# Optimization experiments

Hardware: AMD Instinct MI355X
Metric: run time of the kernel (lower is better)

Reference implementation:

```python
import jax, jax.numpy as jnp
import numpy as np

B, N, D = 4, 1024, 1024
H = 16
DH = D // H  # 64
DROPOUT_P = 0.5


def setup_inputs() -> dict:
    key = jax.random.key(0)
    ks = jax.random.split(key, 6)
    query = jax.random.normal(ks[0], (B, N, D), dtype=jnp.float32)
    key_t = jax.random.normal(ks[1], (B, N, D), dtype=jnp.float32)
    value = jax.random.normal(ks[2], (B, N, D), dtype=jnp.float32)
    # torch Linear(D, 3D): weight [3D, D], bias [3D]
    W_qkv = jax.random.normal(ks[3], (3 * D, D), dtype=jnp.float32) * (1.0 / np.sqrt(D))
    b_qkv = jax.random.normal(ks[4], (3 * D,), dtype=jnp.float32) * 0.01
    # inverted dropout mask: keep_prob = 1 - p, kept entries scaled by 1/keep
    keep = 1.0 - DROPOUT_P
    drop_mask = (jax.random.uniform(ks[5], (B * H, N, N)) < keep).astype(jnp.float32) / keep
    return {"query": query, "key": key_t, "value": value,
            "W_qkv": W_qkv, "b_qkv": b_qkv, "drop_mask": drop_mask}


def _split_heads(t):
    # 'b n (h d) -> (b h) n d'
    b, n, _ = t.shape
    return t.reshape(b, n, H, DH).transpose(0, 2, 1, 3).reshape(b * H, n, DH)


def reference(query, key, value, W_qkv, b_qkv, drop_mask):
    # key/value args are unused by the original module (it derives q,k,v from query)
    qkv = query @ W_qkv.T + b_qkv                      # [b, n, 3d]
    q, k, v = jnp.split(qkv, 3, axis=-1)
    q, k, v = _split_heads(q), _split_heads(k), _split_heads(v)  # [(b h), n, dh]
    qk = jnp.einsum('znd,zmd->znm', q, k)              # [(b h), n, n]
    # faithful quirk: original does qk.div(1/sqrt(dh)) == qk * sqrt(dh)
    scaled_qk = qk * jnp.sqrt(jnp.float32(DH))
    attn = jax.nn.softmax(scaled_qk, axis=-1)
    attn = attn * drop_mask                            # deterministic inverted dropout
    out = jnp.einsum('znm,zmd->znd', attn, v)          # [(b h), n, dh]
    # '(b h) n d -> b n (h d)'
    out = out.reshape(B, H, N, DH).transpose(0, 2, 1, 3).reshape(B, N, D)
    return out
```

## Files before the change

kernel.cpp:

```cpp
#include <hip/hip_runtime.h>


typedef _Float16 f16;
typedef _Float16 f16x4 __attribute__((ext_vector_type(4)));
typedef _Float16 f16x8 __attribute__((ext_vector_type(8)));
typedef float    f32x4 __attribute__((ext_vector_type(4)));

#define MFMA16(a, b, c) __builtin_amdgcn_mfma_f32_16x16x32_f16((a), (b), (c), 0, 0, 0)

__device__ __forceinline__ void gll16(const f16* g, f16* l) {
  __builtin_amdgcn_global_load_lds(
      (const __attribute__((address_space(1))) unsigned int*)g,
      (__attribute__((address_space(3))) unsigned int*)l, 16, 0, 0);
}

__device__ __forceinline__ f16x8 ldsfrag(const f16* tile, int row, int chunk) {
  return *(const f16x8*)&tile[row * 64 + ((chunk ^ (row & 7)) << 3)];
}

__global__ __launch_bounds__(256) void cvt_split(const float4* __restrict__ s,
                                                 f16x4* __restrict__ hi,
                                                 f16x4* __restrict__ lo, int n4) {
  int i = blockIdx.x * 256 + threadIdx.x;
  if (i >= n4) return;
  float4 v = s[i];
  f16x4 h, l;
  h[0] = (f16)v.x; l[0] = (f16)(v.x - (float)h[0]);
  h[1] = (f16)v.y; l[1] = (f16)(v.y - (float)h[1]);
  h[2] = (f16)v.z; l[2] = (f16)(v.z - (float)h[2]);
  h[3] = (f16)v.w; l[3] = (f16)(v.w - (float)h[3]);
  hi[i] = h; lo[i] = l;
}

__global__ __launch_bounds__(256) void proj_gemm(
    const f16* __restrict__ qh, const f16* __restrict__ ql,
    const f16* __restrict__ wh, const f16* __restrict__ wl,
    const float* __restrict__ bias,
    f16* __restrict__ Qh, f16* __restrict__ Ql,
    f16* __restrict__ Kh, f16* __restrict__ Kl,
    f16* __restrict__ Vh) {
  __shared__ f16 Ah[128 * 32], Al[128 * 32], Bh[128 * 32], Bl[128 * 32];
  const int tid = threadIdx.x;
  const int bid = blockIdx.x;
  const int wg = (bid & 7) * 96 + (bid >> 3);
  const int m0 = (wg / 24) * 128, n0 = (wg % 24) * 128;
  const bool isv = (n0 >= 2048);
  const int wid = tid >> 6, lane = tid & 63;
  const int wm = (wid >> 1) * 64, wn = (wid & 1) * 64;
  const int r16 = lane & 15, g = lane >> 4;

  f32x4 zero4 = {0.f, 0.f, 0.f, 0.f};
  f32x4 acc[4][4];
#pragma unroll
  for (int i = 0; i < 4; ++i)
#pragma unroll
    for (int j = 0; j < 4; ++j) acc[i][j] = zero4;

  for (int s = 0; s < 32; ++s) {
    const int kk = s << 5;
    const f16* Abh = qh + (size_t)m0 * 1024 + kk;
    const f16* Abl = ql + (size_t)m0 * 1024 + kk;
    const f16* Bbh = wh + (size_t)n0 * 1024 + kk;
    const f16* Bbl = wl + (size_t)n0 * 1024 + kk;
#pragma unroll
    for (int it = 0; it < 2; ++it) {
      const int c = tid + it * 256;
      const int go = (c >> 2) * 1024 + (c & 3) * 8;
      gll16(Abh + go, &Ah[c * 8]);
      gll16(Bbh + go, &Bh[c * 8]);
      if (!isv) {
        gll16(Abl + go, &Al[c * 8]);
        gll16(Bbl + go, &Bl[c * 8]);
      }
    }
    __syncthreads();
    f16x8 a[4], al_[4];
#pragma unroll
    for (int i = 0; i < 4; ++i) {
      a[i] = *(const f16x8*)&Ah[(wm + i * 16 + r16) * 32 + g * 8];
      if (!isv) al_[i] = *(const f16x8*)&Al[(wm + i * 16 + r16) * 32 + g * 8];
    }
#pragma unroll
    for (int j = 0; j < 4; ++j) {
      const f16x8 b = *(const f16x8*)&Bh[(wn + j * 16 + r16) * 32 + g * 8];
      if (!isv) {
        const f16x8 bl = *(const f16x8*)&Bl[(wn + j * 16 + r16) * 32 + g * 8];
#pragma unroll
        for (int i = 0; i < 4; ++i) {
          acc[i][j] = MFMA16(a[i], b, acc[i][j]);
          acc[i][j] = MFMA16(al_[i], b, acc[i][j]);
          acc[i][j] = MFMA16(a[i], bl, acc[i][j]);
        }
      } else {
#pragma unroll
        for (int i = 0; i < 4; ++i) acc[i][j] = MFMA16(a[i], b, acc[i][j]);
      }
    }
    __syncthreads();
  }

#pragma unroll
  for (int j = 0; j < 4; ++j) {
    const int col = n0 + wn + j * 16 + r16;
    const float bv = bias[col];
#pragma unroll
    for (int i = 0; i < 4; ++i) {
#pragma unroll
      for (int rr = 0; rr < 4; ++rr) {
        const int m = m0 + wm + i * 16 + g * 4 + rr;
        const float c = acc[i][j][rr] + bv;
        const int bi = m >> 10, n = m & 1023;
        if (col < 1024) {
          const int z = bi * 16 + (col >> 6), dh = col & 63;
          const size_t idx = ((size_t)z * 1024 + n) * 64 + dh;
          f16 h = (f16)c;
          Qh[idx] = h; Ql[idx] = (f16)(c - (float)h);
        } else if (col < 2048) {
          const int c2 = col - 1024;
          const int z = bi * 16 + (c2 >> 6), dh = c2 & 63;
          const size_t idx = ((size_t)z * 1024 + n) * 64 + dh;
          f16 h = (f16)c;
          Kh[idx] = h; Kl[idx] = (f16)(c - (float)h);
        } else {
          const int c2 = col - 2048;
          const int z = bi * 16 + (c2 >> 6), dh = c2 & 63;
          Vh[((size_t)z * 1024 + n) * 64 + dh] = (f16)c;
        }
      }
    }
  }
}

__global__ __launch_bounds__(256) void transp_v(const f16* __restrict__ Vh,
                                                f16* __restrict__ Vt) {
  __shared__ f16 t[64][80];
  const int z = blockIdx.y, nt = blockIdx.x;
  const int tid = threadIdx.x;
#pragma unroll
  for (int it = 0; it < 2; ++it) {
    int c = tid + it * 256;
    int row = c >> 3, cc = c & 7;
    *(f16x8*)&t[row][cc * 8] =
        *(const f16x8*)&Vh[(((size_t)z << 10) + nt * 64 + row) * 64 + cc * 8];
  }
  __syncthreads();
#pragma unroll
  for (int it = 0; it < 2; ++it) {
    int c = tid + it * 256;
    int dh = c >> 3, ncc = c & 7;
    f16x8 o;
#pragma unroll
    for (int j = 0; j < 8; ++j) o[j] = t[ncc * 8 + j][dh];
    *(f16x8*)&Vt[((size_t)z * 64 + dh) * 1024 + nt * 64 + ncc * 8] = o;
  }
}

__global__ __launch_bounds__(512) void attn(
    const f16* __restrict__ Qh_, const f16* __restrict__ Ql_,
    const f16* __restrict__ Kh_, const f16* __restrict__ Kl_,
    const f16* __restrict__ Vt_, const float* __restrict__ mask,
    float* __restrict__ out) {
  __shared__ f16 Khs[2][4096], Kls[2][4096], Vts[2][4096];
  __shared__ f16 Ps[8][1024];

  const int bid = blockIdx.x;
  const int wg = (bid & 7) * 64 + (bid >> 3);
  const int qt = wg & 7, z = wg >> 3;
  const int q0 = qt * 128;
  const int tid = threadIdx.x, w = tid >> 6, lane = tid & 63;
  const int r16 = lane & 15, g = lane >> 4;

  const size_t zrow = (size_t)z << 10;
  const f16* qrh = Qh_ + (zrow + q0 + w * 16 + r16) * 64;
  const f16* qrl = Ql_ + (zrow + q0 + w * 16 + r16) * 64;
  f16x8 qa[2], qla[2];
#pragma unroll
  for (int ks = 0; ks < 2; ++ks) {
    qa[ks] = *(const f16x8*)&qrh[ks * 32 + g * 8];
    qla[ks] = *(const f16x8*)&qrl[ks * 32 + g * 8];
  }

  const f16* KzhB = Kh_ + zrow * 64;
  const f16* KzlB = Kl_ + zrow * 64;
  const f16* VzB = Vt_ + (size_t)z * 64 * 1024;
  const int sc = tid, srow = sc >> 3, ssc = ((sc & 7) ^ (srow & 7)) << 3;

#define STAGE(buf, k0_)                                                   \
  do {                                                                    \
    gll16(KzhB + (size_t)((k0_) + srow) * 64 + ssc, &Khs[buf][sc * 8]);   \
    gll16(KzlB + (size_t)((k0_) + srow) * 64 + ssc, &Kls[buf][sc * 8]);   \
    gll16(VzB + (size_t)srow * 1024 + (k0_) + ssc, &Vts[buf][sc * 8]);    \
  } while (0)

  STAGE(0, 0);

  float mrow[4] = {-1e30f, -1e30f, -1e30f, -1e30f};
  float lrow[4] = {0.f, 0.f, 0.f, 0.f};
  f32x4 zero4 = {0.f, 0.f, 0.f, 0.f};
  f32x4 acc[4];
#pragma unroll
  for (int df = 0; df < 4; ++df) acc[df] = zero4;

  const float* mz = mask + ((size_t)z << 20);
  const int qrow_m = q0 + w * 16 + g * 4;
  f16* Pw = &Ps[w][0];
  __syncthreads();

  for (int kt = 0; kt < 16; ++kt) {
    const int cur = kt & 1;
    const int k0 = kt << 6;
    if (kt < 15) STAGE(cur ^ 1, k0 + 64);

    float mv[4][4];
#pragma unroll
    for (int cf = 0; cf < 4; ++cf)
#pragma unroll
      for (int rr = 0; rr < 4; ++rr)
        mv[cf][rr] = mz[(size_t)(qrow_m + rr) * 1024 + k0 + cf * 16 + r16];

    __builtin_amdgcn_s_setprio(1);
    f32x4 s[4];
#pragma unroll
    for (int cf = 0; cf < 4; ++cf) {
      const int krow = cf * 16 + r16;
      const f16x8 kh0 = ldsfrag(&Khs[cur][0], krow, g);
      const f16x8 kh1 = ldsfrag(&Khs[cur][0], krow, 4 + g);
      const f16x8 kl0 = ldsfrag(&Kls[cur][0], krow, g);
      const f16x8 kl1 = ldsfrag(&Kls[cur][0], krow, 4 + g);
      f32x4 t = zero4;
      t = MFMA16(qa[0], kh0, t);
      t = MFMA16(qla[0], kh0, t);
      t = MFMA16(qa[0], kl0, t);
      t = MFMA16(qa[1], kh1, t);
      t = MFMA16(qla[1], kh1, t);
      t = MFMA16(qa[1], kl1, t);
      s[cf] = t;
    }
    __builtin_amdgcn_s_setprio(0);

    float s8[4][4];
#pragma unroll
    for (int cf = 0; cf < 4; ++cf)
#pragma unroll
      for (int rr = 0; rr < 4; ++rr) s8[cf][rr] = s[cf][rr] * 8.0f;

    float rm[4];
#pragma unroll
    for (int rr = 0; rr < 4; ++rr)
      rm[rr] = fmaxf(fmaxf(s8[0][rr], s8[1][rr]), fmaxf(s8[2][rr], s8[3][rr]));
#pragma unroll
    for (int mk = 1; mk < 16; mk <<= 1)
#pragma unroll
      for (int rr = 0; rr < 4; ++rr)
        rm[rr] = fmaxf(rm[rr], __shfl_xor(rm[rr], mk, 64));

    float mnew[4], scal[4];
#pragma unroll
    for (int rr = 0; rr < 4; ++rr) {
      mnew[rr] = fmaxf(mrow[rr], rm[rr]);
      scal[rr] = __expf(mrow[rr] - mnew[rr]);
      mrow[rr] = mnew[rr];
    }

    float p_[4][4], rs[4] = {0.f, 0.f, 0.f, 0.f};
#pragma unroll
    for (int cf = 0; cf < 4; ++cf)
#pragma unroll
      for (int rr = 0; rr < 4; ++rr) {
        p_[cf][rr] = __expf(s8[cf][rr] - mnew[rr]);
        rs[rr] += p_[cf][rr];
      }
#pragma unroll
    for (int mk = 1; mk < 16; mk <<= 1)
#pragma unroll
      for (int rr = 0; rr < 4; ++rr) rs[rr] += __shfl_xor(rs[rr], mk, 64);
#pragma unroll
    for (int rr = 0; rr < 4; ++rr) lrow[rr] = lrow[rr] * scal[rr] + rs[rr];
#pragma unroll
    for (int df = 0; df < 4; ++df)
#pragma unroll
      for (int rr = 0; rr < 4; ++rr) acc[df][rr] *= scal[rr];

#pragma unroll
    for (int cf = 0; cf < 4; ++cf)
#pragma unroll
      for (int rr = 0; rr < 4; ++rr) {
        const int prow = g * 4 + rr, key = cf * 16 + r16;
        Pw[prow * 64 + (((key >> 3) ^ (prow & 7)) << 3) + (key & 7)] =
            (f16)(p_[cf][rr] * mv[cf][rr]);
      }
    f16x8 pf[2];
#pragma unroll
    for (int ks2 = 0; ks2 < 2; ++ks2)
      pf[ks2] = ldsfrag(Pw, r16, ks2 * 4 + g);

    __builtin_amdgcn_s_setprio(1);
#pragma unroll
    for (int df = 0; df < 4; ++df)
#pragma unroll
      for (int ks2 = 0; ks2 < 2; ++ks2)
        acc[df] = MFMA16(pf[ks2],
                         ldsfrag(&Vts[cur][0], df * 16 + r16, ks2 * 4 + g),
                         acc[df]);
    __builtin_amdgcn_s_setprio(0);
    __syncthreads();
  }

  const int bi = z >> 4, hh = z & 15;
#pragma unroll
  for (int df = 0; df < 4; ++df)
#pragma unroll
    for (int rr = 0; rr < 4; ++rr) {
      const int n = q0 + w * 16 + g * 4 + rr;
      out[((size_t)bi * 1024 + n) * 1024 + hh * 64 + df * 16 + r16] =
          acc[df][rr] / lrow[rr];
    }
#undef STAGE
}

extern "C" void kernel_launch(void* const* d_in, const int* in_sizes, int n_in,
                              void* d_out, int out_size, void* d_ws,
                              size_t ws_size, hipStream_t stream) {
  const float* query = (const float*)d_in[0];
  const float* W = (const float*)d_in[3];
  const float* bias = (const float*)d_in[4];
  const float* mask = (const float*)d_in[5];
  float* out = (float*)d_out;

  f16* p = (f16*)d_ws;
  f16* qh = p;              p += (size_t)4096 * 1024;
  f16* ql = p;              p += (size_t)4096 * 1024;
  f16* wh = p;              p += (size_t)3072 * 1024;
  f16* wl = p;              p += (size_t)3072 * 1024;
  f16* Qh = p;              p += (size_t)64 * 1024 * 64;
  f16* Ql = p;              p += (size_t)64 * 1024 * 64;
  f16* Kh = p;              p += (size_t)64 * 1024 * 64;
  f16* Kl = p;              p += (size_t)64 * 1024 * 64;
  f16* Vh = p;              p += (size_t)64 * 1024 * 64;
  f16* Vt = p;

  cvt_split<<<(1048576 + 255) / 256, 256, 0, stream>>>(
      (const float4*)query, (f16x4*)qh, (f16x4*)ql, 1048576);
  cvt_split<<<(786432 + 255) / 256, 256, 0, stream>>>(
      (const float4*)W, (f16x4*)wh, (f16x4*)wl, 786432);
  proj_gemm<<<768, 256, 0, stream>>>(qh, ql, wh, wl, bias, Qh, Ql, Kh, Kl, Vh);
  transp_v<<<dim3(16, 64), 256, 0, stream>>>(Vh, Vt);
  attn<<<512, 512, 0, stream>>>(Qh, Ql, Kh, Kl, Vt, mask, out);
}
```

Baseline: 561.8 us.

## Pack dropout mask to bits and streamline online softmax in attention

A new pre-pass packs the float dropout mask into one bit per element, so the attention kernel reads a single 64-bit word per row per key tile instead of sixteen scattered floats per lane. The QK MFMA operands are swapped so each lane owns a whole query row, which removes most cross-lane shuffles for the row max and row sum. Rescaling of the running max is skipped unless the max grows by more than a threshold, and P is written to LDS as packed 4-wide vectors. The kept value is hardcoded as 2·p, which assumes the mask only holds 0 or 1/keep with keep = 0.5. The full mask is still read once per call, now in a separate extra kernel launch.

```diff
diff --git a/kernel.cpp b/kernel.cpp
--- a/kernel.cpp
+++ b/kernel.cpp
@@ -5,6 +5,8 @@
 typedef _Float16 f16x4 __attribute__((ext_vector_type(4)));
 typedef _Float16 f16x8 __attribute__((ext_vector_type(8)));
 typedef float    f32x4 __attribute__((ext_vector_type(4)));
+typedef unsigned long long u64;
+typedef unsigned short u16;
 
 #define MFMA16(a, b, c) __builtin_amdgcn_mfma_f32_16x16x32_f16((a), (b), (c), 0, 0, 0)
 
@@ -30,6 +32,25 @@
   h[2] = (f16)v.z; l[2] = (f16)(v.z - (float)h[2]);
   h[3] = (f16)v.w; l[3] = (f16)(v.w - (float)h[3]);
   hi[i] = h; lo[i] = l;
+}
+
+__global__ __launch_bounds__(256) void mask_bits(const float4* __restrict__ mask,
+                                                 u16* __restrict__ bits16) {
+  const size_t t = (size_t)blockIdx.x * 256 + threadIdx.x;
+  const float4 v0 = mask[t * 4 + 0];
+  const float4 v1 = mask[t * 4 + 1];
+  const float4 v2 = mask[t * 4 + 2];
+  const float4 v3 = mask[t * 4 + 3];
+  unsigned m = 0;
+  m |= (v0.x > 1.f) ? 0x0001u : 0u;  m |= (v0.y > 1.f) ? 0x0002u : 0u;
+  m |= (v0.z > 1.f) ? 0x0004u : 0u;  m |= (v0.w > 1.f) ? 0x0008u : 0u;
+  m |= (v1.x > 1.f) ? 0x0010u : 0u;  m |= (v1.y > 1.f) ? 0x0020u : 0u;
+  m |= (v1.z > 1.f) ? 0x0040u : 0u;  m |= (v1.w > 1.f) ? 0x0080u : 0u;
+  m |= (v2.x > 1.f) ? 0x0100u : 0u;  m |= (v2.y > 1.f) ? 0x0200u : 0u;
+  m |= (v2.z > 1.f) ? 0x0400u : 0u;  m |= (v2.w > 1.f) ? 0x0800u : 0u;
+  m |= (v3.x > 1.f) ? 0x1000u : 0u;  m |= (v3.y > 1.f) ? 0x2000u : 0u;
+  m |= (v3.z > 1.f) ? 0x4000u : 0u;  m |= (v3.w > 1.f) ? 0x8000u : 0u;
+  bits16[t] = (u16)m;
 }
 
 __global__ __launch_bounds__(256) void proj_gemm(
@@ -158,7 +179,7 @@
 __global__ __launch_bounds__(512) void attn(
     const f16* __restrict__ Qh_, const f16* __restrict__ Ql_,
     const f16* __restrict__ Kh_, const f16* __restrict__ Kl_,
-    const f16* __restrict__ Vt_, const float* __restrict__ mask,
+    const f16* __restrict__ Vt_, const u64* __restrict__ bits,
     float* __restrict__ out) {
   __shared__ f16 Khs[2][4096], Kls[2][4096], Vts[2][4096];
   __shared__ f16 Ps[8][1024];
@@ -194,16 +215,16 @@
 
   STAGE(0, 0);
 
-  float mrow[4] = {-1e30f, -1e30f, -1e30f, -1e30f};
-  float lrow[4] = {0.f, 0.f, 0.f, 0.f};
+  float mrow = -1e30f, lrow = 0.f;
   f32x4 zero4 = {0.f, 0.f, 0.f, 0.f};
   f32x4 acc[4];
 #pragma unroll
   for (int df = 0; df < 4; ++df) acc[df] = zero4;
 
-  const float* mz = mask + ((size_t)z << 20);
-  const int qrow_m = q0 + w * 16 + g * 4;
+  const u64* browp = bits + (zrow + q0 + w * 16 + r16) * 16;
   f16* Pw = &Ps[w][0];
+  f16* pwbase = Pw + r16 * 64 + (g & 1) * 4;
+  const int pswz = r16 & 7, ghalf = g >> 1;
   __syncthreads();
 
   for (int kt = 0; kt < 16; ++kt) {
@@ -211,12 +232,7 @@
     const int k0 = kt << 6;
     if (kt < 15) STAGE(cur ^ 1, k0 + 64);
 
-    float mv[4][4];
-#pragma unroll
-    for (int cf = 0; cf < 4; ++cf)
-#pragma unroll
-      for (int rr = 0; rr < 4; ++rr)
-        mv[cf][rr] = mz[(size_t)(qrow_m + rr) * 1024 + k0 + cf * 16 + r16];
+    const u64 bm = browp[kt];
 
     __builtin_amdgcn_s_setprio(1);
     f32x4 s[4];
@@ -228,12 +244,12 @@
       const f16x8 kl0 = ldsfrag(&Kls[cur][0], krow, g);
       const f16x8 kl1 = ldsfrag(&Kls[cur][0], krow, 4 + g);
       f32x4 t = zero4;
-      t = MFMA16(qa[0], kh0, t);
-      t = MFMA16(qla[0], kh0, t);
-      t = MFMA16(qa[0], kl0, t);
-      t = MFMA16(qa[1], kh1, t);
-      t = MFMA16(qla[1], kh1, t);
-      t = MFMA16(qa[1], kl1, t);
+      t = MFMA16(kh0, qa[0], t);
+      t = MFMA16(kh0, qla[0], t);
+      t = MFMA16(kl0, qa[0], t);
+      t = MFMA16(kh1, qa[1], t);
+      t = MFMA16(kh1, qla[1], t);
+      t = MFMA16(kl1, qa[1], t);
       s[cf] = t;
     }
     __builtin_amdgcn_s_setprio(0);
@@ -244,51 +260,50 @@
 #pragma unroll
       for (int rr = 0; rr < 4; ++rr) s8[cf][rr] = s[cf][rr] * 8.0f;
 
-    float rm[4];
-#pragma unroll
-    for (int rr = 0; rr < 4; ++rr)
-      rm[rr] = fmaxf(fmaxf(s8[0][rr], s8[1][rr]), fmaxf(s8[2][rr], s8[3][rr]));
-#pragma unroll
-    for (int mk = 1; mk < 16; mk <<= 1)
-#pragma unroll
-      for (int rr = 0; rr < 4; ++rr)
-        rm[rr] = fmaxf(rm[rr], __shfl_xor(rm[rr], mk, 64));
-
-    float mnew[4], scal[4];
-#pragma unroll
-    for (int rr = 0; rr < 4; ++rr) {
-      mnew[rr] = fmaxf(mrow[rr], rm[rr]);
-      scal[rr] = __expf(mrow[rr] - mnew[rr]);
-      mrow[rr] = mnew[rr];
-    }
-
-    float p_[4][4], rs[4] = {0.f, 0.f, 0.f, 0.f};
+    float m16 = s8[0][0];
 #pragma unroll
     for (int cf = 0; cf < 4; ++cf)
 #pragma unroll
+      for (int rr = 0; rr < 4; ++rr) m16 = fmaxf(m16, s8[cf][rr]);
+    m16 = fmaxf(m16, __shfl_xor(m16, 16, 64));
+    m16 = fmaxf(m16, __shfl_xor(m16, 32, 64));
+
+    if (!__all(m16 <= mrow + 8.f)) {
+      const float mnew = fmaxf(mrow, m16);
+      const float scal = __expf(mrow - mnew);
+      mrow = mnew;
+      lrow *= scal;
+      float sq[4];
+#pragma unroll
+      for (int rr = 0; rr < 4; ++rr) sq[rr] = __shfl(scal, g * 4 + rr, 16);
+#pragma unroll
+      for (int df = 0; df < 4; ++df)
+#pragma unroll
+        for (int rr = 0; rr < 4; ++rr) acc[df][rr] *= sq[rr];
+    }
+
+    float p_[4][4], rs = 0.f;
+#pragma unroll
+    for (int cf = 0; cf < 4; ++cf)
+#pragma unroll
       for (int rr = 0; rr < 4; ++rr) {
-        p_[cf][rr] = __expf(s8[cf][rr] - mnew[rr]);
-        rs[rr] += p_[cf][rr];
-      }
-#pragma unroll
-    for (int mk = 1; mk < 16; mk <<= 1)
-#pragma unroll
-      for (int rr = 0; rr < 4; ++rr) rs[rr] += __shfl_xor(rs[rr], mk, 64);
-#pragma unroll
-    for (int rr = 0; rr < 4; ++rr) lrow[rr] = lrow[rr] * scal[rr] + rs[rr];
-#pragma unroll
-    for (int df = 0; df < 4; ++df)
-#pragma unroll
-      for (int rr = 0; rr < 4; ++rr) acc[df][rr] *= scal[rr];
-
-#pragma unroll
-    for (int cf = 0; cf < 4; ++cf)
+        p_[cf][rr] = __expf(s8[cf][rr] - mrow);
+        rs += p_[cf][rr];
+      }
+    rs += __shfl_xor(rs, 16, 64);
+    rs += __shfl_xor(rs, 32, 64);
+    lrow += rs;
+
+#pragma unroll
+    for (int cf = 0; cf < 4; ++cf) {
+      f16x4 pk;
 #pragma unroll
       for (int rr = 0; rr < 4; ++rr) {
-        const int prow = g * 4 + rr, key = cf * 16 + r16;
-        Pw[prow * 64 + (((key >> 3) ^ (prow & 7)) << 3) + (key & 7)] =
-            (f16)(p_[cf][rr] * mv[cf][rr]);
-      }
+        const int key = cf * 16 + g * 4 + rr;
+        pk[rr] = ((bm >> key) & 1ull) ? (f16)(p_[cf][rr] + p_[cf][rr]) : (f16)0.f;
+      }
+      *(f16x4*)&pwbase[(((cf * 2 + ghalf) ^ pswz) << 3)] = pk;
+    }
     f16x8 pf[2];
 #pragma unroll
     for (int ks2 = 0; ks2 < 2; ++ks2)
@@ -306,6 +321,10 @@
     __syncthreads();
   }
 
+  const float rl = 1.0f / lrow;
+  float rlq[4];
+#pragma unroll
+  for (int rr = 0; rr < 4; ++rr) rlq[rr] = __shfl(rl, g * 4 + rr, 16);
   const int bi = z >> 4, hh = z & 15;
 #pragma unroll
   for (int df = 0; df < 4; ++df)
@@ -313,7 +332,7 @@
     for (int rr = 0; rr < 4; ++rr) {
       const int n = q0 + w * 16 + g * 4 + rr;
       out[((size_t)bi * 1024 + n) * 1024 + hh * 64 + df * 16 + r16] =
-          acc[df][rr] / lrow[rr];
+          acc[df][rr] * rlq[rr];
     }
 #undef STAGE
 }
@@ -337,13 +356,15 @@
   f16* Kh = p;              p += (size_t)64 * 1024 * 64;
   f16* Kl = p;              p += (size_t)64 * 1024 * 64;
   f16* Vh = p;              p += (size_t)64 * 1024 * 64;
-  f16* Vt = p;
-
+  f16* Vt = p;              p += (size_t)64 * 1024 * 64;
+  u64* bits = (u64*)p;
+
+  mask_bits<<<16384, 256, 0, stream>>>((const float4*)mask, (u16*)bits);
   cvt_split<<<(1048576 + 255) / 256, 256, 0, stream>>>(
       (const float4*)query, (f16x4*)qh, (f16x4*)ql, 1048576);
   cvt_split<<<(786432 + 255) / 256, 256, 0, stream>>>(
       (const float4*)W, (f16x4*)wh, (f16x4*)wl, 786432);
   proj_gemm<<<768, 256, 0, stream>>>(qh, ql, wh, wl, bias, Qh, Ql, Kh, Kl, Vh);
   transp_v<<<dim3(16, 64), 256, 0, stream>>>(Vh, Vt);
-  attn<<<512, 512, 0, stream>>>(Qh, Ql, Kh, Kl, Vt, mask, out);
-}
+  attn<<<512, 512, 0, stream>>>(Qh, Ql, Kh, Kl, Vt, bits, out);
+}
```

New measurement: 568.7 us. No clear change (+1.2%).
